# Kernel tuning notes

Measured on AMD Instinct MI355X. Metric: run time of the kernel, lower is better.

## Reference

```python
import jax, jax.numpy as jnp
import numpy as np

N_SAMPLES, N_ATOMS = 32, 512
IN_DEPTH, OUT_DEPTH, FILTER_LENGTH = 64, 64, 12


def setup_inputs() -> dict:
    key = jax.random.key(0)
    k1, k2, k3, k4 = jax.random.split(key, 4)
    node_property_tensor = jax.random.normal(k1, (N_SAMPLES, N_ATOMS, IN_DEPTH), dtype=jnp.float32)
    # connectivity is conceptually one-hot neighbor selection; random floats suffice for a math baseline
    connectivity_tensor = jax.random.uniform(k2, (N_SAMPLES, N_ATOMS, N_ATOMS, FILTER_LENGTH), dtype=jnp.float32)
    bond_property_tensor = jax.random.normal(k3, (N_SAMPLES, N_ATOMS, FILTER_LENGTH, 2), dtype=jnp.float32)
    # filters init: normal * (1/in_depth/1000), shape (out_depth, filter_length, in_depth+2)
    filters = jax.random.normal(k4, (OUT_DEPTH, FILTER_LENGTH, IN_DEPTH + 2), dtype=jnp.float32) * (1.0 / IN_DEPTH / 1000.0)
    return {
        "node_property_tensor": node_property_tensor,
        "connectivity_tensor": connectivity_tensor,
        "bond_property_tensor": bond_property_tensor,
        "filters": filters,
    }


def reference(node_property_tensor, connectivity_tensor, bond_property_tensor, filters):
    # node_connection[s,a,f,d] = sum_n connectivity[s,a,n,f] * node_prop[s,n,d]
    node_connection = jnp.einsum('sanf,snd->safd', connectivity_tensor, node_property_tensor)
    # append 2 bond properties -> (s, a, f, in_depth+2)
    combined = jnp.concatenate([node_connection, bond_property_tensor], axis=3)
    # out[s,a,o] = sum_{f,d} combined[s,a,f,d] * filters[o,f,d]
    return jnp.einsum('safd,ofd->sao', combined, filters)
```

## Files before the change

kernel.cpp:

```cpp
#include <hip/hip_runtime.h>
#include <hip/hip_bf16.h>
#include <stdint.h>

#define NS 32
#define NA 512
#define IND 64
#define OD 64
#define FL 12
#define KTOT (NA*FL)
#define WROW 66

typedef __bf16 bf16x8 __attribute__((ext_vector_type(8)));
typedef float  f32x4  __attribute__((ext_vector_type(4)));
typedef float  f32x4a __attribute__((ext_vector_type(4), aligned(4)));

__global__ __launch_bounds__(256, 1)
void k_prep(const float* __restrict__ node, const float* __restrict__ W,
            __bf16* __restrict__ gt) {
    const int bid = blockIdx.x;
    const int s  = bid >> 3;
    const int nh = (bid >> 2) & 1;
    const int og = bid & 3;
    const int o0 = og * 16;
    const int nbase = nh * 256;
    const int tid = threadIdx.x;
    const int wv = tid >> 6, l = tid & 63;
    const int lr = l & 15, lg = l >> 4;

    __shared__ __align__(16) unsigned char NodeL[256 * 128];
    __shared__ __align__(16) unsigned char Tr[4][6144];

    bf16x8 afr[FL][2];
    {
        const float* wrow = W + (size_t)(o0 + lr) * (FL * WROW);
        #pragma unroll
        for (int f = 0; f < FL; ++f) {
            #pragma unroll
            for (int kk = 0; kk < 2; ++kk) {
                const float* p = wrow + f * WROW + kk * 32 + lg * 8;
                const f32x4a u0 = *reinterpret_cast<const f32x4a*>(p);
                const f32x4a u1 = *reinterpret_cast<const f32x4a*>(p + 4);
                bf16x8 a;
                a[0] = (__bf16)u0.x; a[1] = (__bf16)u0.y;
                a[2] = (__bf16)u0.z; a[3] = (__bf16)u0.w;
                a[4] = (__bf16)u1.x; a[5] = (__bf16)u1.y;
                a[6] = (__bf16)u1.z; a[7] = (__bf16)u1.w;
                afr[f][kk] = a;
            }
        }
    }

    {
        const f32x4* np = reinterpret_cast<const f32x4*>(
            node + ((size_t)s * NA + nbase) * IND);
        #pragma unroll
        for (int i = 0; i < 16; ++i) {
            const int idx = tid + 256 * i;
            const f32x4 v = np[idx];
            const int n  = idx >> 4;
            const int c8 = idx & 15;
            union { __bf16 b[4]; uint2 u; } cv;
            cv.b[0] = (__bf16)v.x; cv.b[1] = (__bf16)v.y;
            cv.b[2] = (__bf16)v.z; cv.b[3] = (__bf16)v.w;
            const int woff = n * 128 + ((c8 * 8) ^ ((n & 7) << 4));
            *reinterpret_cast<uint2*>(NodeL + woff) = cv.u;
        }
    }
    __syncthreads();

    unsigned char* tr = Tr[wv];
    const int swk = (lr & 7) << 4;
    const int row2 = l >> 2;
    const int rk2 = (row2 & 7) << 4;

    for (int i = 0; i < 4; ++i) {
        const int ln0 = wv * 16 + i * 64;
        f32x4 acc[FL];
        #pragma unroll
        for (int f = 0; f < FL; ++f) acc[f] = f32x4{0.f, 0.f, 0.f, 0.f};

        const int nrow = ln0 + lr;
        #pragma unroll
        for (int kk = 0; kk < 2; ++kk) {
            const int roff = nrow * 128 + (((kk * 4 + lg) * 16) ^ swk);
            const bf16x8 b = *reinterpret_cast<const bf16x8*>(NodeL + roff);
            #pragma unroll
            for (int f = 0; f < FL; ++f)
                acc[f] = __builtin_amdgcn_mfma_f32_16x16x32_bf16(afr[f][kk], b, acc[f], 0, 0, 0);
        }

        #pragma unroll
        for (int r = 0; r < 4; ++r) {
            const int row = 4 * lg + r;
            const int rk = (row & 7) << 4;
            #pragma unroll
            for (int fp = 0; fp < 6; ++fp) {
                union { __bf16 b[2]; uint32_t u; } pk;
                pk.b[0] = (__bf16)acc[2 * fp][r];
                pk.b[1] = (__bf16)acc[2 * fp + 1][r];
                *reinterpret_cast<uint32_t*>(
                    tr + row * 384 + ((lr * 24 + fp * 4) ^ rk)) = pk.u;
            }
        }
        asm volatile("s_waitcnt lgkmcnt(0)" ::: "memory");

        __bf16* gbase = gt + ((size_t)(s * OD + o0 + row2)) * KTOT
                           + (size_t)(nbase + ln0) * FL;
        #pragma unroll
        for (int i6 = 0; i6 < 6; ++i6) {
            const int ch = (l & 3) + 4 * i6;
            const uint4 v = *reinterpret_cast<const uint4*>(
                tr + row2 * 384 + ((ch * 16) ^ rk2));
            reinterpret_cast<uint4*>(gbase)[ch] = v;
        }
        asm volatile("s_waitcnt lgkmcnt(0)" ::: "memory");
    }
}

__global__ __launch_bounds__(256)
void k_init(const float* __restrict__ bond, const float* __restrict__ W,
            float* __restrict__ out) {
    const int bid = blockIdx.x;
    const int tid = threadIdx.x;

    __shared__ float Wb[64][25];
    for (int i = tid; i < 64 * 24; i += 256) {
        const int o = i / 24, fc = i % 24;
        const int f = fc >> 1, c = fc & 1;
        Wb[o][fc] = W[(size_t)o * (FL * WROW) + f * WROW + IND + c];
    }
    __shared__ float bl[4][24];
    if (tid < 96) {
        const int a = tid / 24, fc = tid % 24;
        bl[a][fc] = bond[(size_t)bid * 4 * (FL * 2) + a * (FL * 2) + fc];
    }
    __syncthreads();

    const int aL = tid >> 6, o = tid & 63;
    float sum = 0.f;
    #pragma unroll
    for (int f = 0; f < FL; ++f)
        sum += bl[aL][2 * f] * Wb[o][2 * f] + bl[aL][2 * f + 1] * Wb[o][2 * f + 1];
    out[((size_t)bid * 4 + aL) * OD + o] = sum;
}

struct PF { f32x4 a0, a1, a2, a3; uint4 b0, b1; };

__device__ __forceinline__ PF pf_load(const float* ap, const __bf16* bp) {
    PF p;
    p.a0 = *reinterpret_cast<const f32x4*>(ap);
    p.a1 = *reinterpret_cast<const f32x4*>(ap + 4);
    p.a2 = *reinterpret_cast<const f32x4*>(ap + 8);
    p.a3 = *reinterpret_cast<const f32x4*>(ap + 12);
    p.b0 = *reinterpret_cast<const uint4*>(bp);
    p.b1 = *reinterpret_cast<const uint4*>(bp + 8);
    return p;
}

__device__ __forceinline__ void pf_stage(unsigned char* Ab, unsigned char* Bb,
                                         const PF& p, int woff0, int woff1) {
    bf16x8 wlo, whi;
    wlo[0] = (__bf16)p.a0.x; wlo[1] = (__bf16)p.a0.y;
    wlo[2] = (__bf16)p.a0.z; wlo[3] = (__bf16)p.a0.w;
    wlo[4] = (__bf16)p.a1.x; wlo[5] = (__bf16)p.a1.y;
    wlo[6] = (__bf16)p.a1.z; wlo[7] = (__bf16)p.a1.w;
    whi[0] = (__bf16)p.a2.x; whi[1] = (__bf16)p.a2.y;
    whi[2] = (__bf16)p.a2.z; whi[3] = (__bf16)p.a2.w;
    whi[4] = (__bf16)p.a3.x; whi[5] = (__bf16)p.a3.y;
    whi[6] = (__bf16)p.a3.z; whi[7] = (__bf16)p.a3.w;
    *reinterpret_cast<bf16x8*>(Ab + woff0) = wlo;
    *reinterpret_cast<bf16x8*>(Ab + woff1) = whi;
    *reinterpret_cast<uint4*>(Bb + woff0) = p.b0;
    *reinterpret_cast<uint4*>(Bb + woff1) = p.b1;
}

__device__ __forceinline__ void mfma_phase(const unsigned char* Ab, const unsigned char* Bb,
                                           int rowA0, int rowB0, int lg, int rsw,
                                           f32x4& c00, f32x4& c01, f32x4& c10, f32x4& c11) {
    #pragma unroll
    for (int ks = 0; ks < 2; ++ks) {
        const int koff = (ks * 64 + lg * 16) ^ rsw;
        const bf16x8 am0 = *reinterpret_cast<const bf16x8*>(Ab + rowA0 + koff);
        const bf16x8 am1 = *reinterpret_cast<const bf16x8*>(Ab + rowA0 + 2048 + koff);
        const bf16x8 bn0 = *reinterpret_cast<const bf16x8*>(Bb + rowB0 + koff);
        const bf16x8 bn1 = *reinterpret_cast<const bf16x8*>(Bb + rowB0 + 2048 + koff);
        c00 = __builtin_amdgcn_mfma_f32_16x16x32_bf16(am0, bn0, c00, 0, 0, 0);
        c01 = __builtin_amdgcn_mfma_f32_16x16x32_bf16(am0, bn1, c01, 0, 0, 0);
        c10 = __builtin_amdgcn_mfma_f32_16x16x32_bf16(am1, bn0, c10, 0, 0, 0);
        c11 = __builtin_amdgcn_mfma_f32_16x16x32_bf16(am1, bn1, c11, 0, 0, 0);
    }
}

__global__ __launch_bounds__(256, 4)
void k_main(const float* __restrict__ conn, const __bf16* __restrict__ gt,
            float* __restrict__ out) {
    const int bid = blockIdx.x;
    const int s  = bid & 31;
    const int x  = bid >> 5;
    const int at = x >> 2;
    const int kq = x & 3;
    const int a0 = at << 6;
    const int k00 = kq * (KTOT / 4);
    const int tid = threadIdx.x;
    const int w  = tid >> 6, l = tid & 63;
    const int lr = l & 15, lg = l >> 4;
    const int m0 = (w >> 1) << 5;
    const int n0 = (w & 1) << 5;

    __shared__ __align__(16) unsigned char Al0[8192];
    __shared__ __align__(16) unsigned char Al1[8192];
    __shared__ __align__(16) unsigned char Bl0[8192];
    __shared__ __align__(16) unsigned char Bl1[8192];

    const int srow = tid >> 2;
    const int scol = tid & 3;
    const float*  aG = conn + ((size_t)s * NA + a0 + srow) * KTOT + k00 + scol * 16;
    const __bf16* bG = gt   + ((size_t)s * OD + srow)      * KTOT + k00 + scol * 16;
    const int wsw   = (srow & 7) << 4;
    const int woff0 = srow * 128 + ((scol * 32) ^ wsw);
    const int woff1 = srow * 128 + ((scol * 32 + 16) ^ wsw);

    f32x4 acc00 = {0.f,0.f,0.f,0.f}, acc01 = {0.f,0.f,0.f,0.f};
    f32x4 acc10 = {0.f,0.f,0.f,0.f}, acc11 = {0.f,0.f,0.f,0.f};

    const int rsw = (lr & 7) << 4;
    const int rowA0 = (m0 + lr) * 128;
    const int rowB0 = (n0 + lr) * 128;

    PF P0 = pf_load(aG, bG);
    PF P1 = pf_load(aG + 64, bG + 64);

    #pragma unroll 1
    for (int t = 0; t < 24; t += 2) {
        pf_stage(Al0, Bl0, P0, woff0, woff1);
        if (t + 2 < 24) P0 = pf_load(aG + (t + 2) * 64, bG + (t + 2) * 64);
        asm volatile("s_waitcnt lgkmcnt(0)" ::: "memory");
        __builtin_amdgcn_s_barrier();
        mfma_phase(Al0, Bl0, rowA0, rowB0, lg, rsw, acc00, acc01, acc10, acc11);

        pf_stage(Al1, Bl1, P1, woff0, woff1);
        if (t + 3 < 24) P1 = pf_load(aG + (t + 3) * 64, bG + (t + 3) * 64);
        asm volatile("s_waitcnt lgkmcnt(0)" ::: "memory");
        __builtin_amdgcn_s_barrier();
        mfma_phase(Al1, Bl1, rowA0, rowB0, lg, rsw, acc00, acc01, acc10, acc11);
    }

    float* ob = out + ((size_t)s * NA + a0 + m0 + lg * 4) * OD + n0 + lr;
    #pragma unroll
    for (int r = 0; r < 4; ++r) {
        atomicAdd(ob + (size_t)(r) * OD,            acc00[r]);
        atomicAdd(ob + (size_t)(r) * OD + 16,       acc01[r]);
        atomicAdd(ob + (size_t)(16 + r) * OD,       acc10[r]);
        atomicAdd(ob + (size_t)(16 + r) * OD + 16,  acc11[r]);
    }
}

extern "C" void kernel_launch(void* const* d_in, const int* in_sizes, int n_in,
                              void* d_out, int out_size, void* d_ws, size_t ws_size,
                              hipStream_t stream) {
    const float* node = (const float*)d_in[0];
    const float* conn = (const float*)d_in[1];
    const float* bond = (const float*)d_in[2];
    const float* W    = (const float*)d_in[3];
    float* out = (float*)d_out;
    __bf16* gt = (__bf16*)d_ws;

    k_prep<<<dim3(256), dim3(256), 0, stream>>>(node, W, gt);
    k_init<<<dim3(NS * NA / 4), dim3(256), 0, stream>>>(bond, W, out);
    k_main<<<dim3(NS * 32), dim3(256), 0, stream>>>(conn, gt, out);
}
```

Baseline: 131.0 us.

## Fuse prep and init kernels into one launch with finer prep blocks

Merges the node×filter precompute kernel and the bond-term init kernel into a single launch, with block index choosing which role a block plays. The prep part now uses 512 smaller blocks (128 nodes each) instead of 256, so it needs much less shared memory and can reach higher occupancy. It also drops the LDS transpose staging in favour of direct 8-byte global stores. This removes one kernel launch and the gap between launches, at the cost of less coalesced output stores to the workspace.

```diff
diff --git a/kernel.cpp b/kernel.cpp
--- a/kernel.cpp
+++ b/kernel.cpp
@@ -14,134 +14,115 @@
 typedef float  f32x4  __attribute__((ext_vector_type(4)));
 typedef float  f32x4a __attribute__((ext_vector_type(4), aligned(4)));
 
-__global__ __launch_bounds__(256, 1)
-void k_prep(const float* __restrict__ node, const float* __restrict__ W,
-            __bf16* __restrict__ gt) {
-    const int bid = blockIdx.x;
-    const int s  = bid >> 3;
-    const int nh = (bid >> 2) & 1;
-    const int og = bid & 3;
-    const int o0 = og * 16;
-    const int nbase = nh * 256;
-    const int tid = threadIdx.x;
-    const int wv = tid >> 6, l = tid & 63;
-    const int lr = l & 15, lg = l >> 4;
-
-    __shared__ __align__(16) unsigned char NodeL[256 * 128];
-    __shared__ __align__(16) unsigned char Tr[4][6144];
-
-    bf16x8 afr[FL][2];
-    {
-        const float* wrow = W + (size_t)(o0 + lr) * (FL * WROW);
-        #pragma unroll
-        for (int f = 0; f < FL; ++f) {
-            #pragma unroll
-            for (int kk = 0; kk < 2; ++kk) {
-                const float* p = wrow + f * WROW + kk * 32 + lg * 8;
-                const f32x4a u0 = *reinterpret_cast<const f32x4a*>(p);
-                const f32x4a u1 = *reinterpret_cast<const f32x4a*>(p + 4);
-                bf16x8 a;
-                a[0] = (__bf16)u0.x; a[1] = (__bf16)u0.y;
-                a[2] = (__bf16)u0.z; a[3] = (__bf16)u0.w;
-                a[4] = (__bf16)u1.x; a[5] = (__bf16)u1.y;
-                a[6] = (__bf16)u1.z; a[7] = (__bf16)u1.w;
-                afr[f][kk] = a;
-            }
-        }
-    }
-
-    {
-        const f32x4* np = reinterpret_cast<const f32x4*>(
-            node + ((size_t)s * NA + nbase) * IND);
-        #pragma unroll
-        for (int i = 0; i < 16; ++i) {
-            const int idx = tid + 256 * i;
-            const f32x4 v = np[idx];
-            const int n  = idx >> 4;
-            const int c8 = idx & 15;
-            union { __bf16 b[4]; uint2 u; } cv;
-            cv.b[0] = (__bf16)v.x; cv.b[1] = (__bf16)v.y;
-            cv.b[2] = (__bf16)v.z; cv.b[3] = (__bf16)v.w;
-            const int woff = n * 128 + ((c8 * 8) ^ ((n & 7) << 4));
-            *reinterpret_cast<uint2*>(NodeL + woff) = cv.u;
-        }
-    }
-    __syncthreads();
-
-    unsigned char* tr = Tr[wv];
-    const int swk = (lr & 7) << 4;
-    const int row2 = l >> 2;
-    const int rk2 = (row2 & 7) << 4;
-
-    for (int i = 0; i < 4; ++i) {
-        const int ln0 = wv * 16 + i * 64;
-        f32x4 acc[FL];
-        #pragma unroll
-        for (int f = 0; f < FL; ++f) acc[f] = f32x4{0.f, 0.f, 0.f, 0.f};
-
-        const int nrow = ln0 + lr;
-        #pragma unroll
-        for (int kk = 0; kk < 2; ++kk) {
-            const int roff = nrow * 128 + (((kk * 4 + lg) * 16) ^ swk);
-            const bf16x8 b = *reinterpret_cast<const bf16x8*>(NodeL + roff);
-            #pragma unroll
-            for (int f = 0; f < FL; ++f)
-                acc[f] = __builtin_amdgcn_mfma_f32_16x16x32_bf16(afr[f][kk], b, acc[f], 0, 0, 0);
-        }
-
-        #pragma unroll
-        for (int r = 0; r < 4; ++r) {
-            const int row = 4 * lg + r;
-            const int rk = (row & 7) << 4;
-            #pragma unroll
-            for (int fp = 0; fp < 6; ++fp) {
-                union { __bf16 b[2]; uint32_t u; } pk;
-                pk.b[0] = (__bf16)acc[2 * fp][r];
-                pk.b[1] = (__bf16)acc[2 * fp + 1][r];
-                *reinterpret_cast<uint32_t*>(
-                    tr + row * 384 + ((lr * 24 + fp * 4) ^ rk)) = pk.u;
-            }
-        }
-        asm volatile("s_waitcnt lgkmcnt(0)" ::: "memory");
-
-        __bf16* gbase = gt + ((size_t)(s * OD + o0 + row2)) * KTOT
-                           + (size_t)(nbase + ln0) * FL;
-        #pragma unroll
-        for (int i6 = 0; i6 < 6; ++i6) {
-            const int ch = (l & 3) + 4 * i6;
-            const uint4 v = *reinterpret_cast<const uint4*>(
-                tr + row2 * 384 + ((ch * 16) ^ rk2));
-            reinterpret_cast<uint4*>(gbase)[ch] = v;
-        }
-        asm volatile("s_waitcnt lgkmcnt(0)" ::: "memory");
-    }
-}
-
 __global__ __launch_bounds__(256)
-void k_init(const float* __restrict__ bond, const float* __restrict__ W,
-            float* __restrict__ out) {
+void k_prep_init(const float* __restrict__ node, const float* __restrict__ W,
+                 const float* __restrict__ bond, __bf16* __restrict__ gt,
+                 float* __restrict__ out) {
+    __shared__ __align__(16) unsigned char SMEM[16640];
     const int bid = blockIdx.x;
     const int tid = threadIdx.x;
 
-    __shared__ float Wb[64][25];
-    for (int i = tid; i < 64 * 24; i += 256) {
-        const int o = i / 24, fc = i % 24;
-        const int f = fc >> 1, c = fc & 1;
-        Wb[o][fc] = W[(size_t)o * (FL * WROW) + f * WROW + IND + c];
-    }
-    __shared__ float bl[4][24];
-    if (tid < 96) {
-        const int a = tid / 24, fc = tid % 24;
-        bl[a][fc] = bond[(size_t)bid * 4 * (FL * 2) + a * (FL * 2) + fc];
-    }
-    __syncthreads();
-
-    const int aL = tid >> 6, o = tid & 63;
-    float sum = 0.f;
-    #pragma unroll
-    for (int f = 0; f < FL; ++f)
-        sum += bl[aL][2 * f] * Wb[o][2 * f] + bl[aL][2 * f + 1] * Wb[o][2 * f + 1];
-    out[((size_t)bid * 4 + aL) * OD + o] = sum;
+    if (bid < 512) {
+        const int s  = bid >> 4;
+        const int nq = (bid >> 2) & 3;
+        const int og = bid & 3;
+        const int o0 = og * 16;
+        const int nbase = nq * 128;
+        const int wv = tid >> 6, l = tid & 63;
+        const int lr = l & 15, lg = l >> 4;
+        unsigned char* NodeL = SMEM;
+
+        bf16x8 afr[FL][2];
+        {
+            const float* wrow = W + (size_t)(o0 + lr) * (FL * WROW);
+            #pragma unroll
+            for (int f = 0; f < FL; ++f) {
+                #pragma unroll
+                for (int kk = 0; kk < 2; ++kk) {
+                    const float* p = wrow + f * WROW + kk * 32 + lg * 8;
+                    const f32x4a u0 = *reinterpret_cast<const f32x4a*>(p);
+                    const f32x4a u1 = *reinterpret_cast<const f32x4a*>(p + 4);
+                    bf16x8 a;
+                    a[0] = (__bf16)u0.x; a[1] = (__bf16)u0.y;
+                    a[2] = (__bf16)u0.z; a[3] = (__bf16)u0.w;
+                    a[4] = (__bf16)u1.x; a[5] = (__bf16)u1.y;
+                    a[6] = (__bf16)u1.z; a[7] = (__bf16)u1.w;
+                    afr[f][kk] = a;
+                }
+            }
+        }
+
+        {
+            const f32x4* np = reinterpret_cast<const f32x4*>(
+                node + ((size_t)s * NA + nbase) * IND);
+            #pragma unroll
+            for (int i = 0; i < 8; ++i) {
+                const int idx = tid + 256 * i;
+                const f32x4 v = np[idx];
+                const int n  = idx >> 4;
+                const int c8 = idx & 15;
+                union { __bf16 b[4]; uint2 u; } cv;
+                cv.b[0] = (__bf16)v.x; cv.b[1] = (__bf16)v.y;
+                cv.b[2] = (__bf16)v.z; cv.b[3] = (__bf16)v.w;
+                const int woff = n * 128 + ((c8 * 8) ^ ((n & 7) << 4));
+                *reinterpret_cast<uint2*>(NodeL + woff) = cv.u;
+            }
+        }
+        __syncthreads();
+
+        const int swk = (lr & 7) << 4;
+        #pragma unroll
+        for (int i = 0; i < 2; ++i) {
+            const int ln0 = (wv * 2 + i) * 16;
+            const int nrow = ln0 + lr;
+            f32x4 acc[FL];
+            #pragma unroll
+            for (int f = 0; f < FL; ++f) acc[f] = f32x4{0.f, 0.f, 0.f, 0.f};
+
+            #pragma unroll
+            for (int kk = 0; kk < 2; ++kk) {
+                const int roff = nrow * 128 + (((kk * 4 + lg) * 16) ^ swk);
+                const bf16x8 b = *reinterpret_cast<const bf16x8*>(NodeL + roff);
+                #pragma unroll
+                for (int f = 0; f < FL; ++f)
+                    acc[f] = __builtin_amdgcn_mfma_f32_16x16x32_bf16(afr[f][kk], b, acc[f], 0, 0, 0);
+            }
+
+            #pragma unroll
+            for (int r = 0; r < 4; ++r) {
+                const int o = o0 + 4 * lg + r;
+                const int n = nbase + ln0 + lr;
+                union { __bf16 b[FL]; uint2 u[3]; } pk;
+                #pragma unroll
+                for (int f = 0; f < FL; ++f) pk.b[f] = (__bf16)acc[f][r];
+                uint2* dst = reinterpret_cast<uint2*>(
+                    gt + ((size_t)(s * OD + o)) * KTOT + (size_t)n * FL);
+                dst[0] = pk.u[0]; dst[1] = pk.u[1]; dst[2] = pk.u[2];
+            }
+        }
+    } else {
+        const int ib = bid - 512;
+        float* Wb = reinterpret_cast<float*>(SMEM);
+        float* bl = reinterpret_cast<float*>(SMEM + 6400);
+        for (int i = tid; i < 64 * 24; i += 256) {
+            const int o = i / 24, fc = i % 24;
+            const int f = fc >> 1, c = fc & 1;
+            Wb[o * 25 + fc] = W[(size_t)o * (FL * WROW) + f * WROW + IND + c];
+        }
+        if (tid < 96) {
+            const int a = tid / 24, fc = tid % 24;
+            bl[a * 24 + fc] = bond[(size_t)ib * 4 * (FL * 2) + a * (FL * 2) + fc];
+        }
+        __syncthreads();
+
+        const int aL = tid >> 6, o = tid & 63;
+        float sum = 0.f;
+        #pragma unroll
+        for (int f = 0; f < FL; ++f)
+            sum += bl[aL * 24 + 2 * f] * Wb[o * 25 + 2 * f]
+                 + bl[aL * 24 + 2 * f + 1] * Wb[o * 25 + 2 * f + 1];
+        out[((size_t)ib * 4 + aL) * OD + o] = sum;
+    }
 }
 
 struct PF { f32x4 a0, a1, a2, a3; uint4 b0, b1; };
@@ -265,7 +246,6 @@
     float* out = (float*)d_out;
     __bf16* gt = (__bf16*)d_ws;
 
-    k_prep<<<dim3(256), dim3(256), 0, stream>>>(node, W, gt);
-    k_init<<<dim3(NS * NA / 4), dim3(256), 0, stream>>>(bond, W, out);
+    k_prep_init<<<dim3(512 + NS * NA / 4), dim3(256), 0, stream>>>(node, W, bond, gt, out);
     k_main<<<dim3(NS * 32), dim3(256), 0, stream>>>(conn, gt, out);
 }
```

Measured after the change: 138.9 us. 6.0% more time.
